# Performance work log

Hardware: AMD Instinct MI355X
Metric: run time of the kernel (lower is better)

The kernel has to match this reference:

```python
import jax, jax.numpy as jnp
import numpy as np

H = 8
DK = 32  # head_dim = 256 // 8
SCALE = 1.0 / np.float32(np.sqrt(DK))
EPS = 1e-5


def _ln(x, g, b):
    mu = jnp.mean(x, axis=-1, keepdims=True)
    var = jnp.var(x, axis=-1, keepdims=True)
    return (x - mu) / jnp.sqrt(var + EPS) * g + b


def _lin(x, W, b):
    return x @ W + b


def setup_inputs() -> dict:
    key = jax.random.key(0)
    ks = jax.random.split(key, 16)
    B, M, N, D, F = 4, 64, 512, 256, 1024
    s = 0.02
    inp = {
        "machine_emb": jax.random.normal(ks[0], (B, M, D), jnp.float32),
        "op_emb": jax.random.normal(ks[1], (B, N, D), jnp.float32),
        "edge_emb": jax.random.normal(ks[2], (B, N, M, D), jnp.float32),
        "o2m_mask": jax.random.bernoulli(ks[3], 0.3, (B, N, M)),
    }
    # projection weights stored as (in, out)
    for i, nm in enumerate(["q", "k", "v", "o", "ks", "vs", "e"]):
        inp["W" + nm] = jax.random.normal(ks[4 + i], (D, D), jnp.float32) * s
        inp["b" + nm] = jnp.zeros((D,), jnp.float32)
    # layernorms: norm1 (g1/b1), norm2 (g2/b2), norm_op (gop/bop)
    for nm in ["1", "2", "op"]:
        inp["g" + nm] = jnp.ones((D,), jnp.float32)
        inp["bn" + nm] = jnp.zeros((D,), jnp.float32)
    # FFN
    inp["Wf1"] = jax.random.normal(ks[11], (D, F), jnp.float32) * s
    inp["bf1"] = jnp.zeros((F,), jnp.float32)
    inp["Wf2"] = jax.random.normal(ks[12], (F, D), jnp.float32) * s
    inp["bf2"] = jnp.zeros((D,), jnp.float32)
    return inp


def reference(machine_emb, op_emb, edge_emb, o2m_mask,
              Wq, bq, Wk, bk, Wv, bv, Wo, bo, Wks, bks, Wvs, bvs, We, be,
              g1, bn1, g2, bn2, gop, bnop, Wf1, bf1, Wf2, bf2):
    B, M, D = machine_emb.shape
    N = op_emb.shape[1]

    residual = machine_emb
    machine_norm = _ln(machine_emb, g1, bn1)
    op_norm = _ln(op_emb, gop, bnop)

    # (B, H, M, dk) / (B, H, N, dk)
    q_m = _lin(machine_norm, Wq, bq).reshape(B, M, H, DK).transpose(0, 2, 1, 3)
    k_o = _lin(op_norm, Wk, bk).reshape(B, N, H, DK).transpose(0, 2, 1, 3)
    v_o = _lin(op_norm, Wv, bv).reshape(B, N, H, DK).transpose(0, 2, 1, 3)

    # edge: (B,N,M,D) -> (B,H,M,N,dk)
    edge = _lin(edge_emb, We, be).reshape(B, N, M, H, DK)
    edge = edge.transpose(0, 3, 2, 1, 4)  # bhmnd

    q_total = q_m[:, :, :, None, :] + edge          # (B,H,M,N,dk)
    k_total = k_o[:, :, None, :, :] + edge          # (B,H,M,N,dk)
    v_total = v_o[:, :, None, :, :] + edge          # (B,H,M,N,dk)

    scores = jnp.sum(q_total * k_total, axis=-1) * SCALE  # (B,H,M,N)

    k_self = _lin(machine_norm, Wks, bks).reshape(B, M, H, DK).transpose(0, 2, 1, 3)
    self_scores = jnp.sum(q_m * k_self, axis=-1) * SCALE   # (B,H,M)

    cross_mask = o2m_mask.transpose(0, 2, 1)[:, None, :, :]  # (B,1,M,N)
    combined_scores = jnp.concatenate([self_scores[..., None], scores], axis=-1)  # (B,H,M,1+N)
    self_flag = jnp.ones((B, 1, M, 1), dtype=bool)
    combined_mask = jnp.concatenate([self_flag, jnp.broadcast_to(cross_mask, (B, 1, M, N))], axis=-1)
    combined_scores = jnp.where(combined_mask, combined_scores, -jnp.inf)

    attn = jax.nn.softmax(combined_scores, axis=-1)
    attn = jnp.where(jnp.isnan(attn), 0.0, attn)

    v_self = _lin(machine_norm, Wvs, bvs).reshape(B, M, H, DK).transpose(0, 2, 1, 3)
    combined_values = jnp.concatenate([v_self[:, :, :, None, :], v_total], axis=3)  # (B,H,M,1+N,dk)

    attn_out = jnp.einsum('bhmi,bhmid->bhmd', attn, combined_values)
    attn_out = attn_out.transpose(0, 2, 1, 3).reshape(B, M, D)
    attn_out = _lin(attn_out, Wo, bo)

    machine_emb = residual + attn_out
    h = _ln(machine_emb, g2, bn2)
    ffn = _lin(jax.nn.relu(_lin(h, Wf1, bf1)), Wf2, bf2)
    return machine_emb + ffn
```

## Files before the change

### kernel.cpp

```cpp
#include <hip/hip_runtime.h>
#include <hip/hip_bf16.h>
#include <math.h>

#define H_ 8
#define DK_ 32
#define B_ 4
#define M_ 64
#define N_ 512
#define D_ 256
#define F_ 1024

static constexpr float SCALE = 0.17677669529663687f;
static constexpr float EPS = 1e-5f;

typedef __bf16 bf16x8 __attribute__((ext_vector_type(8)));
typedef float f32x4 __attribute__((ext_vector_type(4)));

__device__ inline float bfbits2f(unsigned int b) {
    union { unsigned int i; float f; } c; c.i = b << 16; return c.f;
}
__device__ inline void unpack8(uint4 u, float* f) {
    f[0] = bfbits2f(u.x & 0xffffu); f[1] = bfbits2f(u.x >> 16);
    f[2] = bfbits2f(u.y & 0xffffu); f[3] = bfbits2f(u.y >> 16);
    f[4] = bfbits2f(u.z & 0xffffu); f[5] = bfbits2f(u.z >> 16);
    f[6] = bfbits2f(u.w & 0xffffu); f[7] = bfbits2f(u.w >> 16);
}

struct TTArgs {
    const void* src[9];
    void* dst[9];
    int tcum[9];
    int kl[9];
    int nl[9];
    const float* bq; const float* bks; const float* bvs; const float* bk; const float* bv;
    float* bqksvs; float* bkv; int* flags;
};

__global__ __launch_bounds__(256) void prep_all(TTArgs a) {
    __shared__ float ld[64][65];
    int bx = blockIdx.x;
    int t = threadIdx.x;
    if (bx >= a.tcum[8]) {
        a.bqksvs[t] = a.bq[t];
        a.bqksvs[256 + t] = a.bks[t];
        a.bqksvs[512 + t] = a.bvs[t];
        a.bkv[t] = a.bk[t];
        a.bkv[256 + t] = a.bv[t];
        if (t == 0) a.flags[1] = 0;
        return;
    }
    int ti = 0;
    while (bx >= a.tcum[ti]) ti++;
    int j = bx - (ti ? a.tcum[ti - 1] : 0);
    int K = 1 << a.kl[ti], N = 1 << a.nl[ti];
    int ntn = N >> 6;
    int kt = j / ntn, nt = j - kt * ntn;
    const float* src = (const float*)a.src[ti];
    __hip_bfloat16* dst = (__hip_bfloat16*)a.dst[ti];
    int col = t & 63, r0 = t >> 6;
#pragma unroll
    for (int i = 0; i < 16; ++i) {
        int r = i * 4 + r0;
        ld[r][col] = src[(size_t)(kt * 64 + r) * N + nt * 64 + col];
    }
    __syncthreads();
#pragma unroll
    for (int i = 0; i < 16; ++i) {
        int r = i * 4 + r0;
        dst[(size_t)(nt * 64 + r) * K + kt * 64 + col] = __float2bfloat16(ld[col][r]);
    }
}

__device__ inline float block_reduce256(float v, bool is_max, float* sbuf) {
#pragma unroll
    for (int off = 32; off > 0; off >>= 1) {
        float o = __shfl_down(v, off, 64);
        v = is_max ? fmaxf(v, o) : (v + o);
    }
    int lane = threadIdx.x & 63, wid = threadIdx.x >> 6;
    if (lane == 0) sbuf[wid] = v;
    __syncthreads();
    float r;
    if (is_max) r = fmaxf(fmaxf(sbuf[0], sbuf[1]), fmaxf(sbuf[2], sbuf[3]));
    else        r = sbuf[0] + sbuf[1] + sbuf[2] + sbuf[3];
    __syncthreads();
    return r;
}

__global__ __launch_bounds__(256) void ln_detect(const float* __restrict__ me,
                                                 const float* __restrict__ oe,
                                                 const float* __restrict__ g1v,
                                                 const float* __restrict__ b1v,
                                                 const float* __restrict__ gov,
                                                 const float* __restrict__ bov,
                                                 __hip_bfloat16* __restrict__ mnorm,
                                                 __hip_bfloat16* __restrict__ onorm,
                                                 const unsigned int* __restrict__ mask,
                                                 int* __restrict__ flags) {
    __shared__ float sbuf[4];
    int bx = blockIdx.x, t = threadIdx.x;
    if (bx >= 2304) {
        uint4 v = ((const uint4*)mask)[(size_t)(bx - 2304) * 256 + t];
        if (v.x > 1u || v.y > 1u || v.z > 1u || v.w > 1u) atomicOr(flags + 1, 1);
        return;
    }
    const float* xin; const float* g; const float* bta; __hip_bfloat16* out; int row;
    if (bx < 256) { xin = me; g = g1v; bta = b1v; out = mnorm; row = bx; }
    else          { xin = oe; g = gov; bta = bov; out = onorm; row = bx - 256; }
    size_t idx = (size_t)row * 256 + t;
    float x = xin[idx];
    float s  = block_reduce256(x, false, sbuf);
    float ss = block_reduce256(x * x, false, sbuf);
    float mu = s * (1.f / 256.f);
    float var = ss * (1.f / 256.f) - mu * mu;
    float y = (x - mu) * rsqrtf(var + EPS) * g[t] + bta[t];
    out[idx] = __float2bfloat16(y);
}

__global__ __launch_bounds__(256) void gemm64_dual(const __hip_bfloat16* __restrict__ A0,
                                                   const __hip_bfloat16* __restrict__ BT0,
                                                   const float* __restrict__ bias0,
                                                   __hip_bfloat16* __restrict__ out0,
                                                   const __hip_bfloat16* __restrict__ A1,
                                                   const __hip_bfloat16* __restrict__ BT1,
                                                   const float* __restrict__ bias1,
                                                   __hip_bfloat16* __restrict__ out1) {
    __shared__ __align__(16) __bf16 As[64 * 40];
    __shared__ __align__(16) __bf16 Bs[64 * 40];
    const int id = blockIdx.x;
    const __hip_bfloat16* A; const __hip_bfloat16* BT; const float* bias;
    __hip_bfloat16* out; int bx, by, ldc;
    if (id < 48) { A = A0; BT = BT0; bias = bias0; out = out0; bx = id & 3;  by = id >> 2; ldc = 768; }
    else { int j = id - 48; A = A1; BT = BT1; bias = bias1; out = out1; bx = j & 31; by = j >> 5; ldc = 512; }
    const int rowBase = bx * 64;
    const int colBase = by * 64;
    const int t = threadIdx.x;
    const int w = t >> 6;
    const int l = t & 63;
    const int lrow = l & 15;
    const int lk8 = (l >> 4) * 8;
    const int ar = t >> 2;
    const int ac = (t & 3) * 8;

    f32x4 acc[4] = {};
    for (int k0 = 0; k0 < 256; k0 += 32) {
        bf16x8 av = *(const bf16x8*)(A + (size_t)(rowBase + ar) * 256 + k0 + ac);
        bf16x8 bv = *(const bf16x8*)(BT + (size_t)(colBase + ar) * 256 + k0 + ac);
        __syncthreads();
        *(bf16x8*)(As + ar * 40 + ac) = av;
        *(bf16x8*)(Bs + ar * 40 + ac) = bv;
        __syncthreads();
        bf16x8 af = *(const bf16x8*)(As + (w * 16 + lrow) * 40 + lk8);
#pragma unroll
        for (int c = 0; c < 4; ++c) {
            bf16x8 bf = *(const bf16x8*)(Bs + (c * 16 + lrow) * 40 + lk8);
            acc[c] = __builtin_amdgcn_mfma_f32_16x16x32_bf16(af, bf, acc[c], 0, 0, 0);
        }
    }
    int rbase = rowBase + w * 16 + ((l >> 4) * 4);
#pragma unroll
    for (int c = 0; c < 4; ++c) {
        int col = colBase + c * 16 + (l & 15);
        float bb = bias[col];
#pragma unroll
        for (int r = 0; r < 4; ++r) {
            int row = rbase + r;
            out[(size_t)row * ldc + col] = __float2bfloat16(acc[c][r] + bb);
        }
    }
}

__global__ __launch_bounds__(256) void edge_gemm4(const float* __restrict__ E,
                                                  const __hip_bfloat16* __restrict__ WeT,
                                                  const float* __restrict__ be,
                                                  const __hip_bfloat16* __restrict__ qkvs,
                                                  const __hip_bfloat16* __restrict__ kov,
                                                  const void* __restrict__ mask,
                                                  const int* __restrict__ flags,
                                                  __hip_bfloat16* __restrict__ eperm,
                                                  float* __restrict__ scT) {
    __shared__ __align__(16) __bf16 smem[64 * 272];
    __bf16* As = smem;
    __bf16* Cs = smem;
    const int bn = blockIdx.x;
    const int b = bn >> 9, n = bn & 511;
    const int t = threadIdx.x;
    const int w = t >> 6;
    const int l = t & 63;
    const int lrow = l & 15;
    const int lk8 = (l >> 4) * 8;
    const int ar = t >> 2;
    const int ac = (t & 3) * 8;
    const float* Ab = E + (size_t)bn * 64 * 256;

    f32x4 acc[4][4] = {};
    for (int k0 = 0; k0 < 256; k0 += 32) {
        const float* ap = Ab + (size_t)ar * 256 + k0 + ac;
        float4 x0 = *(const float4*)ap;
        float4 x1 = *(const float4*)(ap + 4);
        bf16x8 av;
        av[0] = (__bf16)x0.x; av[1] = (__bf16)x0.y; av[2] = (__bf16)x0.z; av[3] = (__bf16)x0.w;
        av[4] = (__bf16)x1.x; av[5] = (__bf16)x1.y; av[6] = (__bf16)x1.z; av[7] = (__bf16)x1.w;
        __syncthreads();
        *(bf16x8*)(As + ar * 40 + ac) = av;
        __syncthreads();
        bf16x8 af[4];
#pragma unroll
        for (int rr = 0; rr < 4; ++rr)
            af[rr] = *(const bf16x8*)(As + (rr * 16 + lrow) * 40 + lk8);
#pragma unroll
        for (int c = 0; c < 4; ++c) {
            bf16x8 bf = *(const bf16x8*)(WeT + (size_t)(w * 64 + c * 16 + lrow) * 256 + k0 + lk8);
#pragma unroll
            for (int rr = 0; rr < 4; ++rr)
                acc[rr][c] = __builtin_amdgcn_mfma_f32_16x16x32_bf16(af[rr], bf, acc[rr][c], 0, 0, 0);
        }
    }
    __syncthreads();
#pragma unroll
    for (int c = 0; c < 4; ++c) {
        int col = w * 64 + c * 16 + (l & 15);
        float bb = be[col];
#pragma unroll
        for (int rr = 0; rr < 4; ++rr) {
#pragma unroll
            for (int r = 0; r < 4; ++r) {
                int m = rr * 16 + (l >> 4) * 4 + r;
                Cs[m * 272 + col] = (__bf16)(acc[rr][c][r] + bb);
            }
        }
    }
    __syncthreads();
    const bool u8 = flags[1] != 0;
    const int seg = t & 31;
    const int h = seg >> 2;
    const int dk8 = (seg & 3) * 8;
#pragma unroll
    for (int j = 0; j < 8; ++j) {
        int m = j * 8 + (t >> 5);
        uint4 ev4 = *(const uint4*)(Cs + m * 272 + seg * 8);
        size_t bhm = (size_t)((b * 8 + h) * 64 + m);
        *(uint4*)(eperm + (bhm * 512 + n) * 32 + dk8) = ev4;
        float ev[8], qf[8], kf[8];
        unpack8(ev4, ev);
        uint4 qv4 = *(const uint4*)(qkvs + (size_t)(b * 64 + m) * 768 + h * 32 + dk8);
        uint4 kv4 = *(const uint4*)(kov + (size_t)(b * 512 + n) * 512 + h * 32 + dk8);
        unpack8(qv4, qf);
        unpack8(kv4, kf);
        float p = 0.f;
#pragma unroll
        for (int i = 0; i < 8; ++i)
            p += (qf[i] + ev[i]) * (kf[i] + ev[i]);
        p += __shfl_xor(p, 1, 64);
        p += __shfl_xor(p, 2, 64);
        if ((t & 3) == 0) {
            int mi = (b * 512 + n) * 64 + m;
            int mk = u8 ? (int)((const unsigned char*)mask)[mi] : ((const int*)mask)[mi];
            scT[(bhm << 9) + n] = mk ? p * SCALE : -__builtin_inff();
        }
    }
}

__global__ __launch_bounds__(256) void smax_attnout(const float* __restrict__ sc,
                                                    const __hip_bfloat16* __restrict__ qkvs,
                                                    const __hip_bfloat16* __restrict__ kov,
                                                    const __hip_bfloat16* __restrict__ eperm,
                                                    __hip_bfloat16* __restrict__ AO) {
    __shared__ float sbuf[4];
    __shared__ float attnS[512];
    __shared__ float selfSc;
    __shared__ float selfA;
    __shared__ float red[16][8];
    int bhm = blockIdx.x;
    int m = bhm & 63;
    int h = (bhm >> 6) & 7;
    int b = bhm >> 9;
    int t = threadIdx.x;
    if (t == 0) {
        const __hip_bfloat16* q  = qkvs + (size_t)(b * 64 + m) * 768 + h * 32;
        const __hip_bfloat16* ks = q + 256;
        float s = 0.f;
        for (int i = 0; i < 32; ++i) s += __bfloat162float(q[i]) * __bfloat162float(ks[i]);
        selfSc = s * SCALE;
    }
    __syncthreads();
    float sv = selfSc;
    float s0 = sc[(size_t)bhm * 512 + t];
    float s1 = sc[(size_t)bhm * 512 + 256 + t];
    float mx = block_reduce256(fmaxf(fmaxf(s0, s1), sv), true, sbuf);
    float e0 = __expf(s0 - mx);
    float e1 = __expf(s1 - mx);
    float eself = __expf(sv - mx);
    float sum = block_reduce256(e0 + e1 + (t == 0 ? eself : 0.f), false, sbuf);
    float inv = 1.f / sum;
    attnS[t] = e0 * inv;
    attnS[256 + t] = e1 * inv;
    if (t == 0) selfA = eself * inv;
    __syncthreads();

    const int d8 = (t & 3) * 8;
    const int ng = t >> 2;
    const int w = t >> 6, l = t & 63;
    const __hip_bfloat16* ebase = eperm + (size_t)bhm * 512 * 32;
    const __hip_bfloat16* vbase = kov + (size_t)(b * 512) * 512 + 256 + h * 32;
    float accv[8] = {};
#pragma unroll
    for (int i = 0; i < 8; ++i) {
        int n = ng + i * 64;
        float a = attnS[n];
        float ev[8], vv[8];
        uint4 e4 = *(const uint4*)(ebase + (size_t)n * 32 + d8);
        uint4 v4 = *(const uint4*)(vbase + (size_t)n * 512 + d8);
        unpack8(e4, ev);
        unpack8(v4, vv);
#pragma unroll
        for (int k = 0; k < 8; ++k) accv[k] += a * (vv[k] + ev[k]);
    }
#pragma unroll
    for (int off = 4; off <= 32; off <<= 1) {
#pragma unroll
        for (int k = 0; k < 8; ++k) accv[k] += __shfl_xor(accv[k], off, 64);
    }
    if ((l >> 2) == 0) {
#pragma unroll
        for (int k = 0; k < 8; ++k) red[w * 4 + (l & 3)][k] = accv[k];
    }
    __syncthreads();
    if (t < 32) {
        int slot = t >> 3, elem = t & 7;
        float r = red[slot][elem] + red[4 + slot][elem] + red[8 + slot][elem] + red[12 + slot][elem];
        float vs = __bfloat162float(qkvs[(size_t)(b * 64 + m) * 768 + 512 + h * 32 + t]);
        r += selfA * vs;
        AO[(size_t)(b * 64 + m) * 256 + h * 32 + t] = __float2bfloat16(r);
    }
}

__global__ __launch_bounds__(256) void oproj_ln(const __hip_bfloat16* __restrict__ AO,
                                                const __hip_bfloat16* __restrict__ WoT,
                                                const float* __restrict__ bo,
                                                const float* __restrict__ resid,
                                                const float* __restrict__ g2,
                                                const float* __restrict__ bn2,
                                                float* __restrict__ m2,
                                                __hip_bfloat16* __restrict__ hn) {
    __shared__ float rowA[256];
    __shared__ float sbuf[4];
    const int r = blockIdx.x;
    const int t = threadIdx.x;
    rowA[t] = __bfloat162float(AO[(size_t)r * 256 + t]);
    __syncthreads();
    float acc = 0.f;
    const __hip_bfloat16* wrow = WoT + (size_t)t * 256;
#pragma unroll
    for (int k0 = 0; k0 < 256; k0 += 8) {
        float wv[8];
        unpack8(*(const uint4*)(wrow + k0), wv);
#pragma unroll
        for (int i = 0; i < 8; ++i) acc += rowA[k0 + i] * wv[i];
    }
    float v = acc + bo[t] + resid[(size_t)r * 256 + t];
    m2[(size_t)r * 256 + t] = v;
    float s  = block_reduce256(v, false, sbuf);
    float ss = block_reduce256(v * v, false, sbuf);
    float mu = s * (1.f / 256.f);
    float var = ss * (1.f / 256.f) - mu * mu;
    float y = (v - mu) * rsqrtf(var + EPS) * g2[t] + bn2[t];
    hn[(size_t)r * 256 + t] = __float2bfloat16(y);
}

__global__ __launch_bounds__(1024) void ffn_fused(const __hip_bfloat16* __restrict__ hn,
                                                  const __hip_bfloat16* __restrict__ Wf1T,
                                                  const float* __restrict__ bf1,
                                                  const __hip_bfloat16* __restrict__ Wf2T,
                                                  const float* __restrict__ bf2,
                                                  const float* __restrict__ m2,
                                                  float* __restrict__ out) {
    __shared__ float rowA[256];
    __shared__ float hrow[4][260];
    const int r = blockIdx.x;
    const int t = threadIdx.x;
    if (t < 256) rowA[t] = __bfloat162float(hn[(size_t)r * 256 + t]);
    __syncthreads();
    {
        float acc = 0.f;
        const __hip_bfloat16* wrow = Wf1T + (size_t)t * 256;
#pragma unroll
        for (int k0 = 0; k0 < 256; k0 += 8) {
            float wv[8];
            unpack8(*(const uint4*)(wrow + k0), wv);
#pragma unroll
            for (int i = 0; i < 8; ++i) acc += rowA[k0 + i] * wv[i];
        }
        hrow[t >> 8][t & 255] = fmaxf(acc + bf1[t], 0.f);
    }
    __syncthreads();
    {
        const int c = t >> 2;
        const int kq = t & 3;
        float acc = 0.f;
        const __hip_bfloat16* wrow = Wf2T + (size_t)c * 1024 + kq * 256;
        const float* hq = hrow[kq];
#pragma unroll
        for (int k0 = 0; k0 < 256; k0 += 8) {
            float wv[8];
            unpack8(*(const uint4*)(wrow + k0), wv);
#pragma unroll
            for (int i = 0; i < 8; ++i) acc += hq[k0 + i] * wv[i];
        }
        acc += __shfl_xor(acc, 1, 64);
        acc += __shfl_xor(acc, 2, 64);
        if (kq == 0)
            out[(size_t)r * 256 + c] = m2[(size_t)r * 256 + c] + bf2[c] + acc;
    }
}

extern "C" void kernel_launch(void* const* d_in, const int* in_sizes, int n_in,
                              void* d_out, int out_size, void* d_ws, size_t ws_size,
                              hipStream_t stream) {
    const float* machine_emb = (const float*)d_in[0];
    const float* op_emb      = (const float*)d_in[1];
    const float* edge_emb    = (const float*)d_in[2];
    const void*  o2m_mask    = d_in[3];

    char* p = (char*)d_ws;
    int* flags = (int*)p;                        p += 256;
    __hip_bfloat16* WqksvsT = (__hip_bfloat16*)p; p += 196608 * 2;
    __hip_bfloat16* WkvT    = (__hip_bfloat16*)p; p += 131072 * 2;
    __hip_bfloat16* WoT     = (__hip_bfloat16*)p; p += 65536 * 2;
    __hip_bfloat16* WeT     = (__hip_bfloat16*)p; p += 65536 * 2;
    __hip_bfloat16* Wf1T    = (__hip_bfloat16*)p; p += 262144 * 2;
    __hip_bfloat16* Wf2T    = (__hip_bfloat16*)p; p += 262144 * 2;
    float* bqksvs           = (float*)p;          p += 768 * 4;
    float* bkv              = (float*)p;          p += 512 * 4;
    __hip_bfloat16* mnorm   = (__hip_bfloat16*)p; p += 65536 * 2;
    __hip_bfloat16* onorm   = (__hip_bfloat16*)p; p += 524288 * 2;
    __hip_bfloat16* qkvs    = (__hip_bfloat16*)p; p += 196608 * 2;
    __hip_bfloat16* kov     = (__hip_bfloat16*)p; p += 1048576 * 2;
    __hip_bfloat16* eperm   = (__hip_bfloat16*)p; p += (size_t)33554432 * 2;
    float* scT       = (float*)p;                p += (size_t)1048576 * 4;
    __hip_bfloat16* AO = (__hip_bfloat16*)p;     p += 65536 * 2;
    float* m2        = (float*)p;                p += 65536 * 4;
    __hip_bfloat16* hn = (__hip_bfloat16*)p;     p += 65536 * 2;

    TTArgs ta;
    const int srcIdx[9] = {4, 12, 14, 6, 8, 10, 16, 24, 26};
    void* dsts[9] = {WqksvsT, WqksvsT + 65536, WqksvsT + 131072,
                     WkvT, WkvT + 65536, WoT, WeT, Wf1T, Wf2T};
    const int kl9[9] = {8, 8, 8, 8, 8, 8, 8, 8, 10};
    const int nl9[9] = {8, 8, 8, 8, 8, 8, 8, 10, 8};
    int tcum = 0;
    for (int i = 0; i < 9; ++i) {
        ta.src[i] = d_in[srcIdx[i]];
        ta.dst[i] = dsts[i];
        int tiles = (1 << (kl9[i] - 6)) * (1 << (nl9[i] - 6));
        tcum += tiles;
        ta.tcum[i] = tcum;
        ta.kl[i] = kl9[i];
        ta.nl[i] = nl9[i];
    }
    ta.bq = (const float*)d_in[5];  ta.bks = (const float*)d_in[13];
    ta.bvs = (const float*)d_in[15]; ta.bk = (const float*)d_in[7];
    ta.bv = (const float*)d_in[9];
    ta.bqksvs = bqksvs; ta.bkv = bkv; ta.flags = flags;

    hipLaunchKernelGGL(prep_all, dim3(tcum + 1), dim3(256), 0, stream, ta);

    hipLaunchKernelGGL(ln_detect, dim3(2336), dim3(256), 0, stream,
                       machine_emb, op_emb,
                       (const float*)d_in[18], (const float*)d_in[19],
                       (const float*)d_in[22], (const float*)d_in[23],
                       mnorm, onorm, (const unsigned int*)o2m_mask, flags);

    hipLaunchKernelGGL(gemm64_dual, dim3(304), dim3(256), 0, stream,
                       mnorm, WqksvsT, bqksvs, qkvs,
                       onorm, WkvT, bkv, kov);

    hipLaunchKernelGGL(edge_gemm4, dim3(2048), dim3(256), 0, stream,
                       edge_emb, WeT, (const float*)d_in[17],
                       qkvs, kov, o2m_mask, flags, eperm, scT);

    hipLaunchKernelGGL(smax_attnout, dim3(2048), dim3(256), 0, stream,
                       scT, qkvs, kov, eperm, AO);

    hipLaunchKernelGGL(oproj_ln, dim3(256), dim3(256), 0, stream,
                       AO, WoT, (const float*)d_in[11], machine_emb,
                       (const float*)d_in[20], (const float*)d_in[21], m2, hn);

    hipLaunchKernelGGL(ffn_fused, dim3(256), dim3(1024), 0, stream,
                       hn, Wf1T, (const float*)d_in[25],
                       Wf2T, (const float*)d_in[27], m2, (float*)d_out);
}
```

Measured before the change: 361.4 us.

## Stage full edge tile into LDS via direct global-to-LDS loads with XOR swizzle

The edge GEMM kernel no longer loads each 32-wide K slice through registers and converts it per iteration with two barriers. It now copies the whole 64x256 fp32 edge tile into 64KB of shared memory up front using buffer global_load_lds, with an XOR swizzle to avoid bank conflicts. The fp32-to-bf16 conversion happens when reading fragments from LDS. This removes the per-iteration syncs and lets all loads be in flight at once, but the 64KB of LDS per block lowers occupancy and the edge data is no longer overlapped with MFMA work within a block.

```diff
diff --git a/kernel.cpp b/kernel.cpp
--- a/kernel.cpp
+++ b/kernel.cpp
@@ -170,7 +170,7 @@
     }
 }
 
-__global__ __launch_bounds__(256) void edge_gemm4(const float* __restrict__ E,
+__global__ __launch_bounds__(256) void edge_gemm7(const float* __restrict__ E,
                                                   const __hip_bfloat16* __restrict__ WeT,
                                                   const float* __restrict__ be,
                                                   const __hip_bfloat16* __restrict__ qkvs,
@@ -179,9 +179,7 @@
                                                   const int* __restrict__ flags,
                                                   __hip_bfloat16* __restrict__ eperm,
                                                   float* __restrict__ scT) {
-    __shared__ __align__(16) __bf16 smem[64 * 272];
-    __bf16* As = smem;
-    __bf16* Cs = smem;
+    __shared__ __align__(16) unsigned char smem[65536];
     const int bn = blockIdx.x;
     const int b = bn >> 9, n = bn & 511;
     const int t = threadIdx.x;
@@ -189,34 +187,52 @@
     const int l = t & 63;
     const int lrow = l & 15;
     const int lk8 = (l >> 4) * 8;
-    const int ar = t >> 2;
-    const int ac = (t & 3) * 8;
-    const float* Ab = E + (size_t)bn * 64 * 256;
-
+    const float* Ab = E + (size_t)bn * (64 * 256);
+
+#pragma unroll
+    for (int j = 0; j < 16; ++j) {
+        int lc = j * 256 + t;
+        int row = lc >> 6;
+        int cc = lc & 63;
+        int sc = cc ^ (row & 7);
+        const float* src = Ab + (((size_t)row << 6) + sc) * 4;
+        unsigned ldsoff = (unsigned)__builtin_amdgcn_readfirstlane((j * 256 + (t & ~63)) * 16);
+        __builtin_amdgcn_global_load_lds(
+            (const __attribute__((address_space(1))) unsigned int*)src,
+            (__attribute__((address_space(3))) unsigned int*)(smem + ldsoff),
+            16, 0, 0);
+    }
+    __syncthreads();
+
+    const float* Es = (const float*)smem;
     f32x4 acc[4][4] = {};
-    for (int k0 = 0; k0 < 256; k0 += 32) {
-        const float* ap = Ab + (size_t)ar * 256 + k0 + ac;
-        float4 x0 = *(const float4*)ap;
-        float4 x1 = *(const float4*)(ap + 4);
-        bf16x8 av;
-        av[0] = (__bf16)x0.x; av[1] = (__bf16)x0.y; av[2] = (__bf16)x0.z; av[3] = (__bf16)x0.w;
-        av[4] = (__bf16)x1.x; av[5] = (__bf16)x1.y; av[6] = (__bf16)x1.z; av[7] = (__bf16)x1.w;
-        __syncthreads();
-        *(bf16x8*)(As + ar * 40 + ac) = av;
-        __syncthreads();
+#pragma unroll
+    for (int kk = 0; kk < 8; ++kk) {
         bf16x8 af[4];
 #pragma unroll
-        for (int rr = 0; rr < 4; ++rr)
-            af[rr] = *(const bf16x8*)(As + (rr * 16 + lrow) * 40 + lk8);
+        for (int rr = 0; rr < 4; ++rr) {
+            int row = rr * 16 + lrow;
+            int c0 = kk * 8 + (l >> 4) * 2;
+            int s0 = c0 ^ (row & 7);
+            int s1 = (c0 + 1) ^ (row & 7);
+            float4 x0 = *(const float4*)(Es + ((size_t)(row << 6) + s0) * 4);
+            float4 x1 = *(const float4*)(Es + ((size_t)(row << 6) + s1) * 4);
+            bf16x8 v;
+            v[0] = (__bf16)x0.x; v[1] = (__bf16)x0.y; v[2] = (__bf16)x0.z; v[3] = (__bf16)x0.w;
+            v[4] = (__bf16)x1.x; v[5] = (__bf16)x1.y; v[6] = (__bf16)x1.z; v[7] = (__bf16)x1.w;
+            af[rr] = v;
+        }
 #pragma unroll
         for (int c = 0; c < 4; ++c) {
-            bf16x8 bf = *(const bf16x8*)(WeT + (size_t)(w * 64 + c * 16 + lrow) * 256 + k0 + lk8);
+            bf16x8 bf = *(const bf16x8*)(WeT + (size_t)(w * 64 + c * 16 + lrow) * 256 + kk * 32 + lk8);
 #pragma unroll
             for (int rr = 0; rr < 4; ++rr)
                 acc[rr][c] = __builtin_amdgcn_mfma_f32_16x16x32_bf16(af[rr], bf, acc[rr][c], 0, 0, 0);
         }
     }
     __syncthreads();
+    __bf16* Cs = (__bf16*)smem;
+
 #pragma unroll
     for (int c = 0; c < 4; ++c) {
         int col = w * 64 + c * 16 + (l & 15);
@@ -475,7 +491,7 @@
                        mnorm, WqksvsT, bqksvs, qkvs,
                        onorm, WkvT, bkv, kov);
 
-    hipLaunchKernelGGL(edge_gemm4, dim3(2048), dim3(256), 0, stream,
+    hipLaunchKernelGGL(edge_gemm7, dim3(2048), dim3(256), 0, stream,
                        edge_emb, WeT, (const float*)d_in[17],
                        qkvs, kov, o2m_mask, flags, eperm, scT);
 
```

New measurement: 380.5 us. 5.3% more time.
